# Kernel optimization log

Measured on AMD Instinct MI355X. Metric: run time of the kernel, lower is better.

## Reference

```python
import jax, jax.numpy as jnp
import numpy as np

B, C, H, W = 4, 256, 64, 64
CQK = C // 16  # 16


def conv2d(x, w, b):
    # x: [B,C,H,W], w: [O,I,3,3], SAME padding, stride 1
    y = jax.lax.conv_general_dilated(
        x, w, window_strides=(1, 1), padding='SAME',
        dimension_numbers=('NCHW', 'OIHW', 'NCHW'))
    return y + b[None, :, None, None]


def setup_inputs() -> dict:
    key = jax.random.key(0)
    ks = jax.random.split(key, 8)
    fan_in = C * 9
    s = 1.0 / np.sqrt(fan_in)
    return {
        'x': jax.random.normal(ks[0], (B, C, H, W), jnp.float32),
        'y': jax.random.normal(ks[1], (B, C, H, W), jnp.float32),
        'wq': jax.random.normal(ks[2], (CQK, C, 3, 3), jnp.float32) * s,
        'bq': jnp.zeros((CQK,), jnp.float32),
        'wk': jax.random.normal(ks[3], (CQK, C, 3, 3), jnp.float32) * s,
        'bk': jnp.zeros((CQK,), jnp.float32),
        'wv': jax.random.normal(ks[4], (C, C, 3, 3), jnp.float32) * s,
        'bv': jnp.zeros((C,), jnp.float32),
    }


def reference(x, y, wq, bq, wk, bk, wv, bv):
    b, c, h, w = x.shape
    n = h * w
    q = conv2d(x, wq, bq).reshape(b, -1, n)            # [B,CQK,N]
    k = conv2d(y, wk, bk).reshape(b, -1, n)            # [B,CQK,N]
    v = conv2d(y, wv, bv).reshape(b, c, n)             # [B,C,N]
    # energy[b,i,j] = sum_d q[b,d,i] * k[b,d,j]  (unscaled, as in source)
    energy = jnp.einsum('bdi,bdj->bij', q, k)          # [B,N,N]
    attn = jax.nn.softmax(energy, axis=-1)
    # out[b,c,i] = sum_j v[b,c,j] * attn[b,i,j]
    out = jnp.einsum('bcj,bij->bci', v, attn)
    return out.reshape(b, c, h, w)
```

## Files before the change

kernel.cpp:

```cpp
#include <hip/hip_runtime.h>
#include <stdint.h>


typedef __bf16 bf16;
typedef bf16 bf16x8 __attribute__((ext_vector_type(8)));
typedef float f32x4 __attribute__((ext_vector_type(4)));
typedef unsigned long long ull;

#define DEV static __device__ __forceinline__

DEV f32x4 mfma16(bf16x8 a, bf16x8 b, f32x4 c) {
  return __builtin_amdgcn_mfma_f32_16x16x32_bf16(a, b, c, 0, 0, 0);
}

#define SMBUF 25344

__global__ void pack_all_kernel(const float* __restrict__ wv, const float* __restrict__ wq,
                                const float* __restrict__ wk, bf16* __restrict__ W3v,
                                bf16* __restrict__ W3q, bf16* __restrict__ W3k) {
  int idx = blockIdx.x * 256 + threadIdx.x;
  if (idx >= 663552) return;
  const float* src;
  bf16* dst;
  int rel, O;
  if (idx < 589824)      { src = wv; dst = W3v; rel = idx; O = 256; }
  else if (idx < 626688) { src = wq; dst = W3q; rel = idx - 589824; O = 16; }
  else                   { src = wk; dst = W3k; rel = idx - 626688; O = 16; }
  int o = rel / 2304, r = rel - o * 2304;
  int ci = r / 9, tap = r - ci * 9;
  int chunk = ci >> 6, c6 = ci & 63;
  int ks = (tap << 1) + (c6 >> 5), j = c6 & 31;
  dst[((chunk * 18 + ks) * O + o) * 32 + j] = (bf16)src[rel];
}

DEV void stage_load(float4* xv, const float* __restrict__ img, int b, int h, int ci0, int t) {
  const int wg = t & 15, clq = t >> 4;
#pragma unroll
  for (int dh = 0; dh < 3; ++dh) {
    int hh = h + dh - 1;
    bool ok = (hh >= 0) && (hh < 64);
#pragma unroll
    for (int cc = 0; cc < 4; ++cc) {
      float4 v = make_float4(0.f, 0.f, 0.f, 0.f);
      if (ok) v = *(const float4*)&img[((((size_t)b << 8) + ci0 + (clq << 2) + cc) * 64 + hh) * 64 + (wg << 2)];
      xv[dh * 4 + cc] = v;
    }
  }
}

DEV void stage_write(char* smc, const float4* xv, int t) {
  if (t < 96) {
    int dh = t >> 5, r = t & 31;
    int wH = (r & 16) ? 65 : 0, cq = r & 15;
    *(ull*)(smc + ((((dh * 66 + wH) << 7) + (cq << 3)) ^ ((wH & 7) << 4))) = 0ull;
  }
  const int wg = t & 15, clq = t >> 4;
#pragma unroll
  for (int dh = 0; dh < 3; ++dh) {
    const float4 a = xv[dh * 4 + 0], b4 = xv[dh * 4 + 1], c4 = xv[dh * 4 + 2], d4 = xv[dh * 4 + 3];
    const float ax[4] = {a.x, a.y, a.z, a.w};
    const float bx[4] = {b4.x, b4.y, b4.z, b4.w};
    const float cx[4] = {c4.x, c4.y, c4.z, c4.w};
    const float dx[4] = {d4.x, d4.y, d4.z, d4.w};
#pragma unroll
    for (int q4 = 0; q4 < 4; ++q4) {
      int wH = (wg << 2) + q4 + 1;
      union { bf16 h4[4]; ull v; } pk;
      pk.h4[0] = (bf16)ax[q4]; pk.h4[1] = (bf16)bx[q4];
      pk.h4[2] = (bf16)cx[q4]; pk.h4[3] = (bf16)dx[q4];
      *(ull*)(smc + ((((dh * 66 + wH) << 7) + (clq << 3)) ^ ((wH & 7) << 4))) = pk.v;
    }
  }
}

__global__ __launch_bounds__(256) void conv_qk_kernel(
    const float* __restrict__ x, const float* __restrict__ y,
    const bf16* __restrict__ W3q, const bf16* __restrict__ W3k,
    const float* __restrict__ bq, const float* __restrict__ bk,
    bf16* __restrict__ qT, bf16* __restrict__ kT) {
  __shared__ __align__(16) char smc[2 * SMBUF];
  const int mode = blockIdx.x >> 8;
  const float* img = mode ? y : x;
  const bf16* W3 = mode ? W3k : W3q;
  const float* bias = mode ? bk : bq;
  const int bi = blockIdx.x & 255;
  const int t = threadIdx.x;
  const int lane = t & 63, wv = t >> 6;
  const int g = lane >> 4, ln = lane & 15;
  const int b = bi >> 6;
  const int h = bi & 63;
  f32x4 acc = {0.f, 0.f, 0.f, 0.f};
  float4 xv[12];
  stage_load(xv, img, b, h, 0, t);
  stage_write(smc, xv, t);
  __syncthreads();
  for (int chunk = 0; chunk < 4; ++chunk) {
    char* cur = smc + (chunk & 1) * SMBUF;
    if (chunk < 3) stage_load(xv, img, b, h, (chunk + 1) << 6, t);
#pragma unroll
    for (int ks = 0; ks < 18; ++ks) {
      const int tap = ks >> 1, clb = (ks & 1) << 5;
      const int kh = tap / 3, kw = tap - kh * 3;
      const int wH = (wv << 4) + ln + kw;
      uint32_t bo = ((((kh * 66 + wH) << 6) + clb + (g << 3)) << 1) ^ ((wH & 7) << 4);
      bf16x8 bfr = *(const bf16x8*)(cur + bo);
      bf16x8 afr = *(const bf16x8*)&W3[(size_t)((chunk * 18 + ks) * 16 + ln) * 32 + (g << 3)];
      acc = mfma16(afr, bfr, acc);
    }
    if (chunk < 3) stage_write(smc + ((chunk + 1) & 1) * SMBUF, xv, t);
    __syncthreads();
  }
  const int p = (h << 6) + (wv << 4) + ln;
#pragma unroll
  for (int r = 0; r < 4; ++r) {
    int o = (g << 2) + r;
    float val = acc[r] + bias[o];
    if (mode == 0) {
      val *= 1.4426950408889634f;
      bf16* drow = qT + (((size_t)b << 12) + p) * 64;
      bf16 hi = (bf16)val;
      drow[o] = hi;
      drow[16 + o] = hi;
      drow[32 + o] = (bf16)(val - (float)hi);
      drow[48 + o] = (bf16)0.f;
    } else {
      bf16* drow = kT + (((size_t)b << 12) + p) * 32;
      bf16 hi = (bf16)val;
      drow[o] = hi;
      drow[16 + o] = (bf16)(val - (float)hi);
    }
  }
}

__global__ __launch_bounds__(256) void conv_v_kernel(
    const float* __restrict__ img, const bf16* __restrict__ W3,
    const float* __restrict__ bias, bf16* __restrict__ VF) {
  __shared__ __align__(16) char smc[SMBUF];
  const int t = threadIdx.x;
  const int lane = t & 63, wv = t >> 6;
  const int g = lane >> 4, ln = lane & 15;
  const int raw = blockIdx.x;
  const int b = raw >> 8;
  const int h = (raw >> 2) & 63;
  const int oh = raw & 3;
  const int obase = (oh << 6) + (wv << 4);
  f32x4 acc[4];
#pragma unroll
  for (int wf = 0; wf < 4; ++wf) acc[wf] = (f32x4){0.f, 0.f, 0.f, 0.f};
  float4 xv[12];
  for (int chunk = 0; chunk < 4; ++chunk) {
    stage_load(xv, img, b, h, chunk << 6, t);
    __syncthreads();
    stage_write(smc, xv, t);
    __syncthreads();
#pragma unroll
    for (int ks = 0; ks < 18; ++ks) {
      const int tap = ks >> 1, clb = (ks & 1) << 5;
      const int kh = tap / 3, kw = tap - kh * 3;
      bf16x8 afr = *(const bf16x8*)&W3[(size_t)((chunk * 18 + ks) * 256 + obase + ln) * 32 + (g << 3)];
#pragma unroll
      for (int wf = 0; wf < 4; ++wf) {
        int wH = (wf << 4) + ln + kw;
        uint32_t bo = ((((kh * 66 + wH) << 6) + clb + (g << 3)) << 1) ^ ((wH & 7) << 4);
        bf16x8 bfr = *(const bf16x8*)(smc + bo);
        acc[wf] = mfma16(afr, bfr, acc[wf]);
      }
    }
  }
  const int cblk = obase >> 4;
#pragma unroll
  for (int r = 0; r < 4; ++r) {
    int c = obase + (g << 2) + r;
    int lnv = c & 15;
    float bvv = bias[c];
#pragma unroll
    for (int wf = 0; wf < 4; ++wf) {
      int p = (h << 6) + (wf << 4) + ln;
      int J = p >> 5, gv = (p >> 3) & 3, e = p & 7;
      VF[(((size_t)(((b << 7) + J) << 4) + cblk) << 9) + (gv << 7) + (lnv << 3) + e] =
          (bf16)(acc[wf][r] + bvv);
    }
  }
}

__global__ __launch_bounds__(512, 2) void attn_kernel(
    const bf16* __restrict__ qT, const bf16* __restrict__ kT,
    const bf16* __restrict__ VF, float* __restrict__ outp) {
  __shared__ __align__(16) char Klds[2 * 4096];
  __shared__ __align__(16) char Plds[2 * 8192];
  __shared__ float lsumS[4][16];
  const int raw = blockIdx.x;
  const int b  = raw & 3;
  const int it = raw >> 2;
  const int i0 = it << 6;
  const int t = threadIdx.x;
  const int lane = t & 63, wv = t >> 6;
  const int g = lane >> 4, ln = lane & 15;
  const bool prod = (wv < 4);
  const int f = wv & 3;
  const int cb = f << 6;
  const int cblk0 = f << 2;

  const char* kTb = (const char*)kT + (((size_t)b << 12) << 6);
  const char* vfb = (const char*)VF + ((size_t)b << 21);

  bf16x8 bq1 = {}, bq2 = {};
  if (prod) {
    const bf16* qrow = &qT[(((size_t)b << 12) + i0 + (f << 4) + ln) * 64];
    bq1 = *(const bf16x8*)&qrow[g << 3];
    bq2 = *(const bf16x8*)&qrow[32 + (g << 3)];
  }
  float lsum = 0.f;
  const int krow = t >> 2, kc = t & 3;
  const uint32_t kwoff = ((uint32_t)krow << 6) + ((uint32_t)(kc ^ (krow & 3)) << 4);

  f32x4 acc[4][4];
#pragma unroll
  for (int cf = 0; cf < 4; ++cf)
#pragma unroll
    for (int ff = 0; ff < 4; ++ff) acc[cf][ff] = (f32x4){0.f, 0.f, 0.f, 0.f};
  bf16x8 avA[8], avB[8];

  if (prod)
    *(f32x4*)(Klds + kwoff) = *(const f32x4*)(kTb + ((size_t)krow << 6) + (kc << 4));
  __syncthreads();

  for (int m = 0; m < 32; ++m) {
    const int jtA = m << 1;
    if (prod) {
      f32x4 s[4];
#pragma unroll
      for (int jf = 0; jf < 4; ++jf) {
        const int row = (jf << 4) + ln;
        bf16x8 ak = *(const bf16x8*)(Klds + ((uint32_t)row << 6) + ((uint32_t)(g ^ (row & 3)) << 4));
        f32x4 z = {0.f, 0.f, 0.f, 0.f};
        s[jf] = mfma16(ak, bq2, mfma16(ak, bq1, z));
      }
#pragma unroll
      for (int jf = 0; jf < 4; ++jf) {
        union { bf16 h[4]; ull v; } pk;
#pragma unroll
        for (int r = 0; r < 4; ++r) {
          float pv = __builtin_amdgcn_exp2f(s[jf][r]);
          lsum += pv;
          pk.h[r] = (bf16)pv;
        }
        uint32_t bo = (((uint32_t)f << 11) + ((uint32_t)ln << 7) + (jf << 5) + (g << 3)) ^ ((ln & 7) << 4);
        *(ull*)(Plds + bo) = pk.v;
      }
      *(f32x4*)(Klds + 4096 + kwoff) =
          *(const f32x4*)(kTb + ((size_t)(((jtA + 1) << 6) + krow) << 6) + (kc << 4));
    } else {
#pragma unroll
      for (int ks = 0; ks < 2; ++ks)
#pragma unroll
        for (int cf = 0; cf < 4; ++cf)
          avB[ks * 4 + cf] = *(const bf16x8*)(vfb +
              ((size_t)(((jtA << 1) + ks) * 16 + cblk0 + cf) << 10) + (lane << 4));
      if (m > 0) {
        __builtin_amdgcn_s_setprio(1);
#pragma unroll
        for (int ks = 0; ks < 2; ++ks) {
          bf16x8 bp[4];
#pragma unroll
          for (int ff = 0; ff < 4; ++ff) {
            uint32_t bo = (8192u + ((uint32_t)ff << 11) + ((uint32_t)ln << 7) + (ks << 6) + (g << 4)) ^ ((ln & 7) << 4);
            bp[ff] = *(const bf16x8*)(Plds + bo);
          }
#pragma unroll
          for (int cf = 0; cf < 4; ++cf)
#pragma unroll
            for (int ff = 0; ff < 4; ++ff)
              acc[cf][ff] = mfma16(avA[ks * 4 + cf], bp[ff], acc[cf][ff]);
        }
        __builtin_amdgcn_s_setprio(0);
      }
    }
    __syncthreads();
    const int jtB = jtA + 1;
    if (prod) {
      f32x4 s[4];
#pragma unroll
      for (int jf = 0; jf < 4; ++jf) {
        const int row = (jf << 4) + ln;
        bf16x8 ak = *(const bf16x8*)(Klds + 4096 + ((uint32_t)row << 6) + ((uint32_t)(g ^ (row & 3)) << 4));
        f32x4 z = {0.f, 0.f, 0.f, 0.f};
        s[jf] = mfma16(ak, bq2, mfma16(ak, bq1, z));
      }
#pragma unroll
      for (int jf = 0; jf < 4; ++jf) {
        union { bf16 h[4]; ull v; } pk;
#pragma unroll
        for (int r = 0; r < 4; ++r) {
          float pv = __builtin_amdgcn_exp2f(s[jf][r]);
          lsum += pv;
          pk.h[r] = (bf16)pv;
        }
        uint32_t bo = (8192u + ((uint32_t)f << 11) + ((uint32_t)ln << 7) + (jf << 5) + (g << 3)) ^ ((ln & 7) << 4);
        *(ull*)(Plds + bo) = pk.v;
      }
      if (m < 31)
        *(f32x4*)(Klds + kwoff) =
            *(const f32x4*)(kTb + ((size_t)(((jtB + 1) << 6) + krow) << 6) + (kc << 4));
    } else {
#pragma unroll
      for (int ks = 0; ks < 2; ++ks)
#pragma unroll
        for (int cf = 0; cf < 4; ++cf)
          avA[ks * 4 + cf] = *(const bf16x8*)(vfb +
              ((size_t)(((jtB << 1) + ks) * 16 + cblk0 + cf) << 10) + (lane << 4));
      __builtin_amdgcn_s_setprio(1);
#pragma unroll
      for (int ks = 0; ks < 2; ++ks) {
        bf16x8 bp[4];
#pragma unroll
        for (int ff = 0; ff < 4; ++ff) {
          uint32_t bo = (((uint32_t)ff << 11) + ((uint32_t)ln << 7) + (ks << 6) + (g << 4)) ^ ((ln & 7) << 4);
          bp[ff] = *(const bf16x8*)(Plds + bo);
        }
#pragma unroll
        for (int cf = 0; cf < 4; ++cf)
#pragma unroll
          for (int ff = 0; ff < 4; ++ff)
            acc[cf][ff] = mfma16(avB[ks * 4 + cf], bp[ff], acc[cf][ff]);
      }
      __builtin_amdgcn_s_setprio(0);
    }
    __syncthreads();
  }
  if (prod) {
    float l = lsum;
    l += __shfl_xor(l, 16, 64);
    l += __shfl_xor(l, 32, 64);
    if (g == 0) lsumS[f][ln] = l;
  } else {
#pragma unroll
    for (int ks = 0; ks < 2; ++ks) {
      bf16x8 bp[4];
#pragma unroll
      for (int ff = 0; ff < 4; ++ff) {
        uint32_t bo = (8192u + ((uint32_t)ff << 11) + ((uint32_t)ln << 7) + (ks << 6) + (g << 4)) ^ ((ln & 7) << 4);
        bp[ff] = *(const bf16x8*)(Plds + bo);
      }
#pragma unroll
      for (int cf = 0; cf < 4; ++cf)
#pragma unroll
        for (int ff = 0; ff < 4; ++ff)
          acc[cf][ff] = mfma16(avA[ks * 4 + cf], bp[ff], acc[cf][ff]);
    }
  }
  __syncthreads();
  if (!prod) {
#pragma unroll
    for (int ff = 0; ff < 4; ++ff) {
      float rdiv = 1.f / lsumS[ff][ln];
      const int i = i0 + (ff << 4) + ln;
#pragma unroll
      for (int cf = 0; cf < 4; ++cf)
#pragma unroll
        for (int r = 0; r < 4; ++r) {
          int c = cb + (cf << 4) + (g << 2) + r;
          outp[(((size_t)b << 8) + c) * 4096 + i] = acc[cf][ff][r] * rdiv;
        }
    }
  }
}

extern "C" void kernel_launch(void* const* d_in, const int* in_sizes, int n_in,
                              void* d_out, int out_size, void* d_ws, size_t ws_size,
                              hipStream_t stream) {
  const float* x  = (const float*)d_in[0];
  const float* y  = (const float*)d_in[1];
  const float* wq = (const float*)d_in[2];
  const float* bq = (const float*)d_in[3];
  const float* wk = (const float*)d_in[4];
  const float* bk = (const float*)d_in[5];
  const float* wv = (const float*)d_in[6];
  const float* bv = (const float*)d_in[7];
  float* out = (float*)d_out;

  char* ws = (char*)d_ws;
  bf16* qT  = (bf16*)(ws);
  bf16* kT  = (bf16*)(ws + (2u << 20));
  bf16* VF  = (bf16*)(ws + (3u << 20));
  bf16* W3v = (bf16*)(ws + (11u << 20));
  bf16* W3q = (bf16*)(ws + (11u << 20) + 1179648u);
  bf16* W3k = (bf16*)(ws + (11u << 20) + 1179648u + 73728u);

  pack_all_kernel<<<2592, 256, 0, stream>>>(wv, wq, wk, W3v, W3q, W3k);
  conv_qk_kernel<<<512, 256, 0, stream>>>(x, y, W3q, W3k, bq, bk, qT, kT);
  conv_v_kernel<<<1024, 256, 0, stream>>>(y, W3v, bv, VF);
  attn_kernel<<<256, 512, 0, stream>>>(qT, kT, VF, out);
}
```

Baseline: 132.9 us.

## Pre-pack y into padded bf16 layout and read conv_v operands from global

Adds a kernel that converts y to bf16 once, in a width-padded, channel-chunked layout. conv_v_kernel then drops its shared-memory staging and both syncthreads per chunk, and loads MFMA B fragments straight from global/L2. This avoids re-staging and re-converting the three input rows in every block, since the four oh blocks share the same rows. In exchange it adds an extra launch and a round trip of the packed tensor through memory, and it relies on the cache to serve repeated, uncoalesced-ish fragment reads.

```diff
diff --git a/kernel.cpp b/kernel.cpp
--- a/kernel.cpp
+++ b/kernel.cpp
@@ -31,6 +31,42 @@
   int chunk = ci >> 6, c6 = ci & 63;
   int ks = (tap << 1) + (c6 >> 5), j = c6 & 31;
   dst[((chunk * 18 + ks) * O + o) * 32 + j] = (bf16)src[rel];
+}
+
+__global__ __launch_bounds__(256) void pack_yF_kernel(
+    const float* __restrict__ y, bf16* __restrict__ yF) {
+  __shared__ __align__(16) char sm[66 * 128];
+  const int t = threadIdx.x;
+  const int raw = blockIdx.x;
+  const int b = raw >> 8, h = (raw >> 2) & 63, chunk = raw & 3;
+  const int wg = t & 15, clq = t >> 4;
+  float4 xv[4];
+#pragma unroll
+  for (int cc = 0; cc < 4; ++cc)
+    xv[cc] = *(const float4*)&y[((((size_t)b << 8) + (chunk << 6) + (clq << 2) + cc) * 64 + h) * 64 + (wg << 2)];
+  const float xs0[4] = {xv[0].x, xv[0].y, xv[0].z, xv[0].w};
+  const float xs1[4] = {xv[1].x, xv[1].y, xv[1].z, xv[1].w};
+  const float xs2[4] = {xv[2].x, xv[2].y, xv[2].z, xv[2].w};
+  const float xs3[4] = {xv[3].x, xv[3].y, xv[3].z, xv[3].w};
+#pragma unroll
+  for (int q4 = 0; q4 < 4; ++q4) {
+    int wH = (wg << 2) + q4 + 1;
+    union { bf16 h4[4]; ull v; } pk;
+    pk.h4[0] = (bf16)xs0[q4]; pk.h4[1] = (bf16)xs1[q4];
+    pk.h4[2] = (bf16)xs2[q4]; pk.h4[3] = (bf16)xs3[q4];
+    *(ull*)(sm + (((wH << 7) + (clq << 3)) ^ ((wH & 7) << 4))) = pk.v;
+  }
+  __syncthreads();
+  ull* dst = (ull*)yF + (size_t)(((b * 64 + h) * 4 + chunk) * 2) * 66 * 8;
+  for (int idx = t; idx < 1056; idx += 256) {
+    int half = (idx >= 528) ? 1 : 0;
+    int rem = idx - half * 528;
+    int wH = rem >> 3, gr = rem & 7;
+    ull v = 0;
+    if (wH != 0 && wH != 65)
+      v = *(const ull*)(sm + (((wH << 7) + (half << 6) + (gr << 3)) ^ ((wH & 7) << 4)));
+    dst[(size_t)(half * 66 + wH) * 8 + gr] = v;
+  }
 }
 
 DEV void stage_load(float4* xv, const float* __restrict__ img, int b, int h, int ci0, int t) {
@@ -133,9 +169,8 @@
 }
 
 __global__ __launch_bounds__(256) void conv_v_kernel(
-    const float* __restrict__ img, const bf16* __restrict__ W3,
+    const bf16* __restrict__ yF, const bf16* __restrict__ W3,
     const float* __restrict__ bias, bf16* __restrict__ VF) {
-  __shared__ __align__(16) char smc[SMBUF];
   const int t = threadIdx.x;
   const int lane = t & 63, wv = t >> 6;
   const int g = lane >> 4, ln = lane & 15;
@@ -147,23 +182,25 @@
   f32x4 acc[4];
 #pragma unroll
   for (int wf = 0; wf < 4; ++wf) acc[wf] = (f32x4){0.f, 0.f, 0.f, 0.f};
-  float4 xv[12];
   for (int chunk = 0; chunk < 4; ++chunk) {
-    stage_load(xv, img, b, h, chunk << 6, t);
-    __syncthreads();
-    stage_write(smc, xv, t);
-    __syncthreads();
-#pragma unroll
-    for (int ks = 0; ks < 18; ++ks) {
-      const int tap = ks >> 1, clb = (ks & 1) << 5;
-      const int kh = tap / 3, kw = tap - kh * 3;
-      bf16x8 afr = *(const bf16x8*)&W3[(size_t)((chunk * 18 + ks) * 256 + obase + ln) * 32 + (g << 3)];
-#pragma unroll
-      for (int wf = 0; wf < 4; ++wf) {
-        int wH = (wf << 4) + ln + kw;
-        uint32_t bo = ((((kh * 66 + wH) << 6) + clb + (g << 3)) << 1) ^ ((wH & 7) << 4);
-        bf16x8 bfr = *(const bf16x8*)(smc + bo);
-        acc[wf] = mfma16(afr, bfr, acc[wf]);
+#pragma unroll
+    for (int kh = 0; kh < 3; ++kh) {
+      const int hh = h + kh - 1;
+      if (hh < 0 || hh > 63) continue;
+      const char* yb = (const char*)yF + (size_t)(((b * 64 + hh) * 4 + chunk) * 2) * (66 * 64);
+#pragma unroll
+      for (int kw = 0; kw < 3; ++kw) {
+#pragma unroll
+        for (int half = 0; half < 2; ++half) {
+          const int ks = ((kh * 3 + kw) << 1) + half;
+          bf16x8 afr = *(const bf16x8*)&W3[(size_t)((chunk * 18 + ks) * 256 + obase + ln) * 32 + (g << 3)];
+          const char* yrow = yb + (size_t)half * (66 * 64) + (size_t)(ln + kw) * 64 + (g << 4);
+#pragma unroll
+          for (int wf = 0; wf < 4; ++wf) {
+            bf16x8 bfr = *(const bf16x8*)(yrow + (wf << 10));
+            acc[wf] = mfma16(afr, bfr, acc[wf]);
+          }
+        }
       }
     }
   }
@@ -386,9 +423,11 @@
   bf16* W3v = (bf16*)(ws + (11u << 20));
   bf16* W3q = (bf16*)(ws + (11u << 20) + 1179648u);
   bf16* W3k = (bf16*)(ws + (11u << 20) + 1179648u + 73728u);
+  bf16* yF  = (bf16*)(ws + (13u << 20));
 
   pack_all_kernel<<<2592, 256, 0, stream>>>(wv, wq, wk, W3v, W3q, W3k);
+  pack_yF_kernel<<<1024, 256, 0, stream>>>(y, yF);
   conv_qk_kernel<<<512, 256, 0, stream>>>(x, y, W3q, W3k, bq, bk, qT, kT);
-  conv_v_kernel<<<1024, 256, 0, stream>>>(y, W3v, bv, VF);
+  conv_v_kernel<<<1024, 256, 0, stream>>>(yF, W3v, bv, VF);
   attn_kernel<<<256, 512, 0, stream>>>(qT, kT, VF, out);
 }
```

New measurement: 174.8 us. 31.6% more time.
